# Kernel tuning notes

Hardware: AMD Instinct MI355X
Metric: run time of the kernel (lower is better)

Reference implementation:

```python
import jax, jax.numpy as jnp
import numpy as np

N_ORI = 20        # number of origin (dataset-specific) classes
IGNORE_INDEX = 255


def setup_inputs() -> dict:
    key = jax.random.key(0)
    k1, k2 = jax.random.split(key)
    B, C_UNI, H, W = 4, 64, 512, 512
    inputs = jax.random.normal(k1, (B, C_UNI, H, W), dtype=jnp.float32)
    targets = jax.random.randint(k2, (B, H, W), 0, N_ORI).astype(jnp.int64)
    # origin_id for each unified channel; arange % N_ORI guarantees every
    # origin class owns at least one unified channel (no empty groups -> no log(0))
    group_ids = (jnp.arange(C_UNI) % N_ORI).astype(jnp.int32)
    return {"inputs": inputs, "targets": targets, "group_ids": group_ids}


def reference(inputs, targets, group_ids):
    # global-max-shifted exp, as in the torch code (single scalar max)
    max_ = inputs.max()
    e = jnp.exp(inputs - max_)                     # [B, C_uni, H, W]
    # segment-reduce unified channels into origin classes (select_from_uniid)
    e_cfirst = jnp.moveaxis(e, 1, 0)               # [C_uni, B, H, W]
    ori = jax.ops.segment_sum(e_cfirst, group_ids, num_segments=N_ORI)
    ori = jnp.moveaxis(ori, 0, 1)                  # [B, C_ori, H, W]
    # s = ori / sum_over_all_unified;  logp = log(s)
    logp = jnp.log(ori) - jnp.log(e.sum(axis=1, keepdims=True))
    # NLLLoss(ignore_index=255, reduction='mean')
    mask = targets != IGNORE_INDEX                 # [B, H, W]
    safe_t = jnp.where(mask, targets, 0)
    picked = jnp.take_along_axis(logp, safe_t[:, None, :, :], axis=1)[:, 0]
    n_valid = jnp.maximum(mask.sum(), 1)
    loss = -jnp.where(mask, picked, 0.0).sum() / n_valid
    return loss
```

## Files before the change

kernel.cpp:

```cpp
#include <hip/hip_runtime.h>

#define B_      4
#define C_UNI   64
#define H_      512
#define W_      512
#define HW      (H_ * W_)
#define HW_LOG2 18
#define N_PIX   (B_ * HW)
#define NBLOCKS 2048
#define IGNORE_INDEX 255

typedef float f32x2 __attribute__((ext_vector_type(2)));


__global__ __launch_bounds__(256, 8) void uni_ce_main(
    const float* __restrict__ inp,
    const int*   __restrict__ targets,
    const int*   __restrict__ gids,
    float2*      __restrict__ partial)
{
    __shared__ int s_gid[C_UNI];
    const int tid = threadIdx.x;
    if (tid < C_UNI) s_gid[tid] = gids[tid];
    __syncthreads();

    const int g    = blockIdx.x * blockDim.x + tid;
    const int base = g << 1;
    const int b    = base >> HW_LOG2;
    const int pix  = base & (HW - 1);

    const int2 t2 = *(const int2*)(targets + base);

    const float* p = inp + (((size_t)(b * C_UNI)) << HW_LOG2) + pix;

    float den0 = 0.f, den1 = 0.f, num0 = 0.f, num1 = 0.f;

    #pragma unroll 8
    for (int c = 0; c < C_UNI; ++c) {
        const f32x2 x = *(const f32x2*)(p + ((size_t)c << HW_LOG2));
        const float e0 = __expf(x.x);
        const float e1 = __expf(x.y);
        den0 += e0;
        den1 += e1;
        const int gc = s_gid[c];
        if (gc == t2.x) num0 += e0;
        if (gc == t2.y) num1 += e1;
    }

    float loss = 0.f, cnt = 0.f;
    if (t2.x != IGNORE_INDEX) { loss += __logf(den0) - __logf(num0); cnt += 1.f; }
    if (t2.y != IGNORE_INDEX) { loss += __logf(den1) - __logf(num1); cnt += 1.f; }

    #pragma unroll
    for (int off = 32; off > 0; off >>= 1) {
        loss += __shfl_down(loss, off);
        cnt  += __shfl_down(cnt,  off);
    }

    __shared__ float s_loss[4];
    __shared__ float s_cnt[4];
    const int wave = tid >> 6;
    const int lane = tid & 63;
    if (lane == 0) { s_loss[wave] = loss; s_cnt[wave] = cnt; }
    __syncthreads();
    if (tid == 0) {
        float2 pr;
        pr.x = s_loss[0] + s_loss[1] + s_loss[2] + s_loss[3];
        pr.y = s_cnt[0]  + s_cnt[1]  + s_cnt[2]  + s_cnt[3];
        partial[blockIdx.x] = pr;
    }
}

__global__ __launch_bounds__(256) void uni_ce_final(
    const float2* __restrict__ partial,
    float*        __restrict__ out)
{
    const int tid = threadIdx.x;
    const float4 q0 = *(const float4*)(partial + tid * 8);
    const float4 q1 = *(const float4*)(partial + tid * 8 + 2);
    const float4 q2 = *(const float4*)(partial + tid * 8 + 4);
    const float4 q3 = *(const float4*)(partial + tid * 8 + 6);
    float loss = q0.x + q0.z + q1.x + q1.z + q2.x + q2.z + q3.x + q3.z;
    float cnt  = q0.y + q0.w + q1.y + q1.w + q2.y + q2.w + q3.y + q3.w;

    #pragma unroll
    for (int off = 32; off > 0; off >>= 1) {
        loss += __shfl_down(loss, off);
        cnt  += __shfl_down(cnt,  off);
    }

    __shared__ float s_loss[4];
    __shared__ float s_cnt[4];
    const int wave = tid >> 6;
    const int lane = tid & 63;
    if (lane == 0) { s_loss[wave] = loss; s_cnt[wave] = cnt; }
    __syncthreads();
    if (tid == 0) {
        const float L = s_loss[0] + s_loss[1] + s_loss[2] + s_loss[3];
        const float C = s_cnt[0]  + s_cnt[1]  + s_cnt[2]  + s_cnt[3];
        out[0] = L / fmaxf(C, 1.0f);
    }
}

extern "C" void kernel_launch(void* const* d_in, const int* in_sizes, int n_in,
                              void* d_out, int out_size, void* d_ws, size_t ws_size,
                              hipStream_t stream) {
    const float* inp = (const float*)d_in[0];
    const int*   tgt = (const int*)d_in[1];
    const int*   gid = (const int*)d_in[2];
    float* out = (float*)d_out;
    float2* partial = (float2*)d_ws;

    const int threads = 256;
    uni_ce_main<<<NBLOCKS, threads, 0, stream>>>(inp, tgt, gid, partial);
    uni_ce_final<<<1, threads, 0, stream>>>(partial, out);
}
```

Before: 359.7 us.

## Process 8 pixels per thread with 16-byte nontemporal loads and software prefetch

Each thread now handles two float4 groups of pixels (8 pixels) instead of a float2 pair. Channel loads are nontemporal 16-byte loads, and the next channel is loaded one iteration ahead with the loop kept rolled (unroll 1). The block grows to 512 threads and covers 4096 pixels, giving 256 blocks, so the final kernel reads one partial per thread. The intent is wider memory transactions and less cache pollution on a bandwidth-bound stream. The risks are fewer blocks in flight and reduced memory-level parallelism from only one channel of lookahead.

Measured after the change: 338.4 us. 5.9% less time.

```diff
diff --git a/kernel.cpp b/kernel.cpp
--- a/kernel.cpp
+++ b/kernel.cpp
@@ -7,13 +7,18 @@
 #define HW      (H_ * W_)
 #define HW_LOG2 18
 #define N_PIX   (B_ * HW)
-#define NBLOCKS 2048
 #define IGNORE_INDEX 255
 
-typedef float f32x2 __attribute__((ext_vector_type(2)));
+#define TILE_PX 4096
+#define NBLOCKS (N_PIX / TILE_PX)
+#define THREADS 512
+
+typedef float f32x4 __attribute__((ext_vector_type(4)));
+
+#define NT_LOAD(ptr) __builtin_nontemporal_load((const f32x4*)(ptr))
 
 
-__global__ __launch_bounds__(256, 8) void uni_ce_main(
+__global__ __launch_bounds__(THREADS) void uni_ce_main(
     const float* __restrict__ inp,
     const int*   __restrict__ targets,
     const int*   __restrict__ gids,
@@ -24,32 +29,79 @@
     if (tid < C_UNI) s_gid[tid] = gids[tid];
     __syncthreads();
 
-    const int g    = blockIdx.x * blockDim.x + tid;
-    const int base = g << 1;
-    const int b    = base >> HW_LOG2;
-    const int pix  = base & (HW - 1);
-
-    const int2 t2 = *(const int2*)(targets + base);
+    const int tilepx = blockIdx.x * TILE_PX;
+    const int b      = tilepx >> HW_LOG2;
+    const int pix    = tilepx & (HW - 1);
 
     const float* p = inp + (((size_t)(b * C_UNI)) << HW_LOG2) + pix;
 
-    float den0 = 0.f, den1 = 0.f, num0 = 0.f, num1 = 0.f;
+    const int e0 = tid * 4;
+    const int e1 = 2048 + tid * 4;
 
-    #pragma unroll 8
-    for (int c = 0; c < C_UNI; ++c) {
-        const f32x2 x = *(const f32x2*)(p + ((size_t)c << HW_LOG2));
-        const float e0 = __expf(x.x);
-        const float e1 = __expf(x.y);
-        den0 += e0;
-        den1 += e1;
+    const int4 tg0 = *(const int4*)(targets + tilepx + e0);
+    const int4 tg1 = *(const int4*)(targets + tilepx + e1);
+
+    float den0x = 0.f, den0y = 0.f, den0z = 0.f, den0w = 0.f;
+    float den1x = 0.f, den1y = 0.f, den1z = 0.f, den1w = 0.f;
+    float num0x = 0.f, num0y = 0.f, num0z = 0.f, num0w = 0.f;
+    float num1x = 0.f, num1y = 0.f, num1z = 0.f, num1w = 0.f;
+
+    f32x4 cur0 = NT_LOAD(p + e0);
+    f32x4 cur1 = NT_LOAD(p + e1);
+
+    #pragma unroll 1
+    for (int c = 0; c < C_UNI - 1; ++c) {
+        const float* pn = p + (((size_t)(c + 1)) << HW_LOG2);
+        const f32x4 nxt0 = NT_LOAD(pn + e0);
+        const f32x4 nxt1 = NT_LOAD(pn + e1);
+
         const int gc = s_gid[c];
-        if (gc == t2.x) num0 += e0;
-        if (gc == t2.y) num1 += e1;
+
+        const float a0 = __expf(cur0.x), a1 = __expf(cur0.y),
+                    a2 = __expf(cur0.z), a3 = __expf(cur0.w);
+        const float b0 = __expf(cur1.x), b1 = __expf(cur1.y),
+                    b2 = __expf(cur1.z), b3 = __expf(cur1.w);
+        den0x += a0; den0y += a1; den0z += a2; den0w += a3;
+        den1x += b0; den1y += b1; den1z += b2; den1w += b3;
+        if (gc == tg0.x) num0x += a0;
+        if (gc == tg0.y) num0y += a1;
+        if (gc == tg0.z) num0z += a2;
+        if (gc == tg0.w) num0w += a3;
+        if (gc == tg1.x) num1x += b0;
+        if (gc == tg1.y) num1y += b1;
+        if (gc == tg1.z) num1z += b2;
+        if (gc == tg1.w) num1w += b3;
+
+        cur0 = nxt0;
+        cur1 = nxt1;
+    }
+    {
+        const int gc = s_gid[C_UNI - 1];
+        const float a0 = __expf(cur0.x), a1 = __expf(cur0.y),
+                    a2 = __expf(cur0.z), a3 = __expf(cur0.w);
+        const float b0 = __expf(cur1.x), b1 = __expf(cur1.y),
+                    b2 = __expf(cur1.z), b3 = __expf(cur1.w);
+        den0x += a0; den0y += a1; den0z += a2; den0w += a3;
+        den1x += b0; den1y += b1; den1z += b2; den1w += b3;
+        if (gc == tg0.x) num0x += a0;
+        if (gc == tg0.y) num0y += a1;
+        if (gc == tg0.z) num0z += a2;
+        if (gc == tg0.w) num0w += a3;
+        if (gc == tg1.x) num1x += b0;
+        if (gc == tg1.y) num1y += b1;
+        if (gc == tg1.z) num1z += b2;
+        if (gc == tg1.w) num1w += b3;
     }
 
     float loss = 0.f, cnt = 0.f;
-    if (t2.x != IGNORE_INDEX) { loss += __logf(den0) - __logf(num0); cnt += 1.f; }
-    if (t2.y != IGNORE_INDEX) { loss += __logf(den1) - __logf(num1); cnt += 1.f; }
+    if (tg0.x != IGNORE_INDEX) { loss += __logf(den0x) - __logf(num0x); cnt += 1.f; }
+    if (tg0.y != IGNORE_INDEX) { loss += __logf(den0y) - __logf(num0y); cnt += 1.f; }
+    if (tg0.z != IGNORE_INDEX) { loss += __logf(den0z) - __logf(num0z); cnt += 1.f; }
+    if (tg0.w != IGNORE_INDEX) { loss += __logf(den0w) - __logf(num0w); cnt += 1.f; }
+    if (tg1.x != IGNORE_INDEX) { loss += __logf(den1x) - __logf(num1x); cnt += 1.f; }
+    if (tg1.y != IGNORE_INDEX) { loss += __logf(den1y) - __logf(num1y); cnt += 1.f; }
+    if (tg1.z != IGNORE_INDEX) { loss += __logf(den1z) - __logf(num1z); cnt += 1.f; }
+    if (tg1.w != IGNORE_INDEX) { loss += __logf(den1w) - __logf(num1w); cnt += 1.f; }
 
     #pragma unroll
     for (int off = 32; off > 0; off >>= 1) {
@@ -57,16 +109,18 @@
         cnt  += __shfl_down(cnt,  off);
     }
 
-    __shared__ float s_loss[4];
-    __shared__ float s_cnt[4];
+    __shared__ float s_loss[8];
+    __shared__ float s_cnt[8];
     const int wave = tid >> 6;
     const int lane = tid & 63;
     if (lane == 0) { s_loss[wave] = loss; s_cnt[wave] = cnt; }
     __syncthreads();
     if (tid == 0) {
         float2 pr;
-        pr.x = s_loss[0] + s_loss[1] + s_loss[2] + s_loss[3];
-        pr.y = s_cnt[0]  + s_cnt[1]  + s_cnt[2]  + s_cnt[3];
+        pr.x = s_loss[0] + s_loss[1] + s_loss[2] + s_loss[3]
+             + s_loss[4] + s_loss[5] + s_loss[6] + s_loss[7];
+        pr.y = s_cnt[0] + s_cnt[1] + s_cnt[2] + s_cnt[3]
+             + s_cnt[4] + s_cnt[5] + s_cnt[6] + s_cnt[7];
         partial[blockIdx.x] = pr;
     }
 }
@@ -76,12 +130,9 @@
     float*        __restrict__ out)
 {
     const int tid = threadIdx.x;
-    const float4 q0 = *(const float4*)(partial + tid * 8);
-    const float4 q1 = *(const float4*)(partial + tid * 8 + 2);
-    const float4 q2 = *(const float4*)(partial + tid * 8 + 4);
-    const float4 q3 = *(const float4*)(partial + tid * 8 + 6);
-    float loss = q0.x + q0.z + q1.x + q1.z + q2.x + q2.z + q3.x + q3.z;
-    float cnt  = q0.y + q0.w + q1.y + q1.w + q2.y + q2.w + q3.y + q3.w;
+    const float2 q = partial[tid];
+    float loss = q.x;
+    float cnt  = q.y;
 
     #pragma unroll
     for (int off = 32; off > 0; off >>= 1) {
@@ -111,7 +162,6 @@
     float* out = (float*)d_out;
     float2* partial = (float2*)d_ws;
 
-    const int threads = 256;
-    uni_ce_main<<<NBLOCKS, threads, 0, stream>>>(inp, tgt, gid, partial);
-    uni_ce_final<<<1, threads, 0, stream>>>(partial, out);
+    uni_ce_main<<<NBLOCKS, THREADS, 0, stream>>>(inp, tgt, gid, partial);
+    uni_ce_final<<<1, 256, 0, stream>>>(partial, out);
 }
```

## Use 16-byte nontemporal loads with register prefetch over channels

Applied to the files above, without the earlier changes.

Each thread now processes four pixels with 128-bit nontemporal loads and keeps a four-deep register prefetch of upcoming channels in a rolled loop. Blocks grow to 512 threads covering 2048 pixels, so there are fewer blocks and the final reduction reads one partial per thread. The intent is to cut the number of memory instructions and keep more bytes in flight to approach streaming bandwidth. The cost is fewer blocks per CU and a shallower explicit prefetch than the previous unrolled loop might have allowed.

Measured after the change: 332.8 us. 1.08x faster.

```diff
diff --git a/kernel.cpp b/kernel.cpp
--- a/kernel.cpp
+++ b/kernel.cpp
@@ -7,13 +7,19 @@
 #define HW      (H_ * W_)
 #define HW_LOG2 18
 #define N_PIX   (B_ * HW)
-#define NBLOCKS 2048
 #define IGNORE_INDEX 255
 
-typedef float f32x2 __attribute__((ext_vector_type(2)));
+#define TILE_PX 2048
+#define NBLOCKS (N_PIX / TILE_PX)
+#define THREADS 512
+#define PF      4
+
+typedef float f32x4 __attribute__((ext_vector_type(4)));
+
+#define NT_LOAD(ptr) __builtin_nontemporal_load((const f32x4*)(ptr))
 
 
-__global__ __launch_bounds__(256, 8) void uni_ce_main(
+__global__ __launch_bounds__(THREADS, 4) void uni_ce_main(
     const float* __restrict__ inp,
     const int*   __restrict__ targets,
     const int*   __restrict__ gids,
@@ -24,32 +30,53 @@
     if (tid < C_UNI) s_gid[tid] = gids[tid];
     __syncthreads();
 
-    const int g    = blockIdx.x * blockDim.x + tid;
-    const int base = g << 1;
-    const int b    = base >> HW_LOG2;
-    const int pix  = base & (HW - 1);
+    const int tilepx = blockIdx.x * TILE_PX;
+    const int b      = tilepx >> HW_LOG2;
+    const int pix    = tilepx & (HW - 1);
+    const int e      = tid * 4;
 
-    const int2 t2 = *(const int2*)(targets + base);
+    const int4 tg = *(const int4*)(targets + tilepx + e);
 
-    const float* p = inp + (((size_t)(b * C_UNI)) << HW_LOG2) + pix;
+    const float* p = inp + (((size_t)(b * C_UNI)) << HW_LOG2) + pix + e;
 
-    float den0 = 0.f, den1 = 0.f, num0 = 0.f, num1 = 0.f;
+    float denx = 0.f, deny = 0.f, denz = 0.f, denw = 0.f;
+    float numx = 0.f, numy = 0.f, numz = 0.f, numw = 0.f;
 
-    #pragma unroll 8
-    for (int c = 0; c < C_UNI; ++c) {
-        const f32x2 x = *(const f32x2*)(p + ((size_t)c << HW_LOG2));
-        const float e0 = __expf(x.x);
-        const float e1 = __expf(x.y);
-        den0 += e0;
-        den1 += e1;
-        const int gc = s_gid[c];
-        if (gc == t2.x) num0 += e0;
-        if (gc == t2.y) num1 += e1;
+    f32x4 b0 = NT_LOAD(p + ((size_t)0 << HW_LOG2));
+    f32x4 b1 = NT_LOAD(p + ((size_t)1 << HW_LOG2));
+    f32x4 b2 = NT_LOAD(p + ((size_t)2 << HW_LOG2));
+    f32x4 b3 = NT_LOAD(p + ((size_t)3 << HW_LOG2));
+
+    #define PROCESS(vec, gc_)                                            \
+    {                                                                    \
+        const int   gc = (gc_);                                          \
+        const float a0 = __expf((vec).x), a1 = __expf((vec).y),          \
+                    a2 = __expf((vec).z), a3 = __expf((vec).w);          \
+        denx += a0; deny += a1; denz += a2; denw += a3;                  \
+        if (gc == tg.x) numx += a0;                                      \
+        if (gc == tg.y) numy += a1;                                      \
+        if (gc == tg.z) numz += a2;                                      \
+        if (gc == tg.w) numw += a3;                                      \
     }
 
+    #pragma unroll 1
+    for (int c = 0; c < C_UNI - PF; c += PF) {
+        { f32x4 cur = b0; b0 = NT_LOAD(p + ((size_t)(c + 0 + PF) << HW_LOG2)); PROCESS(cur, s_gid[c + 0]); }
+        { f32x4 cur = b1; b1 = NT_LOAD(p + ((size_t)(c + 1 + PF) << HW_LOG2)); PROCESS(cur, s_gid[c + 1]); }
+        { f32x4 cur = b2; b2 = NT_LOAD(p + ((size_t)(c + 2 + PF) << HW_LOG2)); PROCESS(cur, s_gid[c + 2]); }
+        { f32x4 cur = b3; b3 = NT_LOAD(p + ((size_t)(c + 3 + PF) << HW_LOG2)); PROCESS(cur, s_gid[c + 3]); }
+    }
+    PROCESS(b0, s_gid[C_UNI - 4]);
+    PROCESS(b1, s_gid[C_UNI - 3]);
+    PROCESS(b2, s_gid[C_UNI - 2]);
+    PROCESS(b3, s_gid[C_UNI - 1]);
+    #undef PROCESS
+
     float loss = 0.f, cnt = 0.f;
-    if (t2.x != IGNORE_INDEX) { loss += __logf(den0) - __logf(num0); cnt += 1.f; }
-    if (t2.y != IGNORE_INDEX) { loss += __logf(den1) - __logf(num1); cnt += 1.f; }
+    if (tg.x != IGNORE_INDEX) { loss += __logf(denx) - __logf(numx); cnt += 1.f; }
+    if (tg.y != IGNORE_INDEX) { loss += __logf(deny) - __logf(numy); cnt += 1.f; }
+    if (tg.z != IGNORE_INDEX) { loss += __logf(denz) - __logf(numz); cnt += 1.f; }
+    if (tg.w != IGNORE_INDEX) { loss += __logf(denw) - __logf(numw); cnt += 1.f; }
 
     #pragma unroll
     for (int off = 32; off > 0; off >>= 1) {
@@ -57,31 +84,30 @@
         cnt  += __shfl_down(cnt,  off);
     }
 
-    __shared__ float s_loss[4];
-    __shared__ float s_cnt[4];
+    __shared__ float s_loss[8];
+    __shared__ float s_cnt[8];
     const int wave = tid >> 6;
     const int lane = tid & 63;
     if (lane == 0) { s_loss[wave] = loss; s_cnt[wave] = cnt; }
     __syncthreads();
     if (tid == 0) {
         float2 pr;
-        pr.x = s_loss[0] + s_loss[1] + s_loss[2] + s_loss[3];
-        pr.y = s_cnt[0]  + s_cnt[1]  + s_cnt[2]  + s_cnt[3];
+        pr.x = s_loss[0] + s_loss[1] + s_loss[2] + s_loss[3]
+             + s_loss[4] + s_loss[5] + s_loss[6] + s_loss[7];
+        pr.y = s_cnt[0] + s_cnt[1] + s_cnt[2] + s_cnt[3]
+             + s_cnt[4] + s_cnt[5] + s_cnt[6] + s_cnt[7];
         partial[blockIdx.x] = pr;
     }
 }
 
-__global__ __launch_bounds__(256) void uni_ce_final(
+__global__ __launch_bounds__(512) void uni_ce_final(
     const float2* __restrict__ partial,
     float*        __restrict__ out)
 {
     const int tid = threadIdx.x;
-    const float4 q0 = *(const float4*)(partial + tid * 8);
-    const float4 q1 = *(const float4*)(partial + tid * 8 + 2);
-    const float4 q2 = *(const float4*)(partial + tid * 8 + 4);
-    const float4 q3 = *(const float4*)(partial + tid * 8 + 6);
-    float loss = q0.x + q0.z + q1.x + q1.z + q2.x + q2.z + q3.x + q3.z;
-    float cnt  = q0.y + q0.w + q1.y + q1.w + q2.y + q2.w + q3.y + q3.w;
+    const float2 q = partial[tid];
+    float loss = q.x;
+    float cnt  = q.y;
 
     #pragma unroll
     for (int off = 32; off > 0; off >>= 1) {
@@ -89,15 +115,17 @@
         cnt  += __shfl_down(cnt,  off);
     }
 
-    __shared__ float s_loss[4];
-    __shared__ float s_cnt[4];
+    __shared__ float s_loss[8];
+    __shared__ float s_cnt[8];
     const int wave = tid >> 6;
     const int lane = tid & 63;
     if (lane == 0) { s_loss[wave] = loss; s_cnt[wave] = cnt; }
     __syncthreads();
     if (tid == 0) {
-        const float L = s_loss[0] + s_loss[1] + s_loss[2] + s_loss[3];
-        const float C = s_cnt[0]  + s_cnt[1]  + s_cnt[2]  + s_cnt[3];
+        const float L = s_loss[0] + s_loss[1] + s_loss[2] + s_loss[3]
+                      + s_loss[4] + s_loss[5] + s_loss[6] + s_loss[7];
+        const float C = s_cnt[0] + s_cnt[1] + s_cnt[2] + s_cnt[3]
+                      + s_cnt[4] + s_cnt[5] + s_cnt[6] + s_cnt[7];
         out[0] = L / fmaxf(C, 1.0f);
     }
 }
@@ -111,7 +139,6 @@
     float* out = (float*)d_out;
     float2* partial = (float2*)d_ws;
 
-    const int threads = 256;
-    uni_ce_main<<<NBLOCKS, threads, 0, stream>>>(inp, tgt, gid, partial);
-    uni_ce_final<<<1, threads, 0, stream>>>(partial, out);
+    uni_ce_main<<<NBLOCKS, THREADS, 0, stream>>>(inp, tgt, gid, partial);
+    uni_ce_final<<<1, 512, 0, stream>>>(partial, out);
 }
```
